# Kernel tuning notes

Measured on AMD Instinct MI355X. Metric: run time of the kernel, lower is better.

## Reference

```python
import jax, jax.numpy as jnp
import numpy as np

NUM_TASKS = 5
POOL = 5
R = 8
TOPK = 3
SCALE = 1.0  # module self.scale and forward scale arg, both 1
B, S, DIN, DOUT = 4, 4096, 1024, 1024


def setup_inputs() -> dict:
    key = jax.random.key(0)
    ks = jax.random.split(key, 5)
    inp = {
        "input": jax.random.normal(ks[0], (B, S, DIN), dtype=jnp.float32),
        "W": jax.random.normal(ks[1], (DOUT, DIN), dtype=jnp.float32) / np.sqrt(DIN),
        "lora_down": jax.random.normal(ks[2], (POOL, DIN, R), dtype=jnp.float32) / np.sqrt(DIN),
        "lora_up": jax.random.normal(ks[3], (POOL, R, DOUT), dtype=jnp.float32) / np.sqrt(R),
        "lora_route": jax.random.normal(ks[4], (NUM_TASKS, DIN, POOL), dtype=jnp.float32) * 0.02,
        "task_id": 4,
    }
    return inp


def reference(input, W, lora_down, lora_up, lora_route, task_id):
    # Eval branch (self.training == False), 1 <= task_id <= num_tasks.
    task_id = min(task_id, NUM_TASKS)
    k = min(task_id, TOPK)
    route = lora_route[1]                          # [DIN, POOL] (detach split is a no-op for fwd)
    input_mean = jnp.mean(input, axis=1)           # [B, DIN]
    lora_omegas = jnp.mean(input_mean @ route, axis=0)  # [POOL]
    sliced = lora_omegas[1:task_id + 1]            # source slices from 1
    G, I = jax.lax.top_k(sliced, k)                # indices used DIRECTLY (as in source)
    gate = jax.nn.softmax(G)                       # [k]
    # detached expert products (eval path detaches lora_down @ lora_up)
    dw = jax.lax.stop_gradient(
        jnp.einsum('kdr,kro->kdo', lora_down[I], lora_up[I]))  # [k, DIN, DOUT]
    # delta = sum_i gate[i] * SCALE * (input @ dw[i]); forward scale arg = 1
    delta = SCALE * jnp.einsum('k,bsd,kdo->bso', gate, input, dw)
    # delta_w_all[:B//2] = 0
    bmask = (jnp.arange(input.shape[0]) >= input.shape[0] // 2).astype(delta.dtype)
    delta = delta * bmask[:, None, None]
    return input @ W.T + delta
```

## Files before the change

### kernel.cpp

```cpp
#include <hip/hip_runtime.h>
#include <hip/hip_bf16.h>

typedef __attribute__((ext_vector_type(8))) __bf16 bf16x8;
typedef __attribute__((ext_vector_type(4))) __bf16 bf16x4;
typedef __attribute__((ext_vector_type(4))) float f32x4;

#define DIN 1024
#define DOUT 1024
#define BB 4
#define SS 4096
#define MROWS (BB*SS)
#define POOLN 5
#define RR 8
#define NTASKS 5
#define TOPKK 3

__global__ __launch_bounds__(256) void k1a_stream(const float* __restrict__ in,
                                                  __bf16* __restrict__ inB,
                                                  float* __restrict__ partial) {
    const int t = threadIdx.x;
    const int b = blockIdx.x;
    const int tid = b * 256 + t;
    const f32x4* __restrict__ inv = (const f32x4*)in;
    bf16x4* __restrict__ outv = (bf16x4*)inB;

    float s0 = 0.f, s1 = 0.f, s2 = 0.f, s3 = 0.f;
    size_t ia = (size_t)tid;
    size_t ib = (size_t)tid + 2097152;
    f32x4 ca = __builtin_nontemporal_load(&inv[ia]);
    f32x4 cb = __builtin_nontemporal_load(&inv[ib]);
#pragma unroll
    for (int i = 0; i < 4; ++i) {
        f32x4 na = ca, nb = cb;
        if (i < 3) {
            na = __builtin_nontemporal_load(&inv[ia + 524288]);
            nb = __builtin_nontemporal_load(&inv[ib + 524288]);
        }
        s0 += ca[0] + cb[0]; s1 += ca[1] + cb[1];
        s2 += ca[2] + cb[2]; s3 += ca[3] + cb[3];
        bf16x4 oa = { (__bf16)ca[0], (__bf16)ca[1], (__bf16)ca[2], (__bf16)ca[3] };
        bf16x4 ob = { (__bf16)cb[0], (__bf16)cb[1], (__bf16)cb[2], (__bf16)cb[3] };
        outv[ia] = oa;
        outv[ib] = ob;
        ca = na; cb = nb;
        ia += 524288; ib += 524288;
    }
    const int c0 = (t * 4) & (DIN - 1);
    f32x4 p = { s0, s1, s2, s3 };
    *(f32x4*)&partial[(size_t)b * DIN + c0] = p;
}

__global__ __launch_bounds__(256) void k1b_reduce(const float* __restrict__ partial,
                                                  float* __restrict__ partial2) {
    const int tid = blockIdx.x * 256 + threadIdx.x;
    const int c = tid & (DIN - 1);
    const int g = tid >> 10;
    float s = 0.f;
    const int r0 = g * 256;
#pragma unroll 8
    for (int r = r0; r < r0 + 256; ++r)
        s += partial[(size_t)r * DIN + c];
    partial2[(size_t)g * DIN + c] = s;
}

__global__ void k2_gate(const float* __restrict__ partial2,
                        const float* __restrict__ lroute,
                        const int* __restrict__ task_id_p,
                        float* __restrict__ gate, int* __restrict__ gidx) {
    __shared__ float red[4][POOLN];
    const int tix = threadIdx.x;
    const int w = tix >> 6, l = tix & 63;
    float part[POOLN] = {0.f, 0.f, 0.f, 0.f, 0.f};
    for (int d = w * 256 + l; d < w * 256 + 256; d += 64) {
        float cs = 0.f;
#pragma unroll
        for (int g = 0; g < 8; ++g) cs += partial2[g * DIN + d];
        cs *= (1.0f / (float)MROWS);
        const float* rp = &lroute[(size_t)1 * DIN * POOLN + (size_t)d * POOLN];
#pragma unroll
        for (int p = 0; p < POOLN; ++p) part[p] += cs * rp[p];
    }
#pragma unroll
    for (int p = 0; p < POOLN; ++p) {
        float v = part[p];
        for (int off = 32; off; off >>= 1) v += __shfl_down(v, off);
        if (l == 0) red[w][p] = v;
    }
    __syncthreads();
    if (tix == 0) {
#pragma unroll
        for (int p = 0; p < POOLN; ++p)
            part[p] = red[0][p] + red[1][p] + red[2][p] + red[3][p];
        int tid = *task_id_p;
        if (tid > NTASKS) tid = NTASKS;
        int L = tid < (POOLN - 1) ? tid : (POOLN - 1);
        int k = tid < TOPKK ? tid : TOPKK;
        float sl[POOLN];
        for (int j = 0; j < L; ++j) sl[j] = part[1 + j];
        float G[TOPKK]; int I[TOPKK];
        int used = 0;
        for (int j = 0; j < k; ++j) {
            int best = -1; float bv = 0.f;
            for (int i2 = 0; i2 < L; ++i2) {
                if (used & (1 << i2)) continue;
                if (best < 0 || sl[i2] > bv) { bv = sl[i2]; best = i2; }
            }
            used |= 1 << best; G[j] = bv; I[j] = best;
        }
        if (k > 0) {
            float m = G[0];
            float e[TOPKK]; float se = 0.f;
            for (int j = 0; j < k; ++j) { e[j] = expf(G[j] - m); se += e[j]; }
            for (int j = 0; j < k; ++j) { gate[j] = e[j] / se; gidx[j] = I[j]; }
        }
        for (int j = k; j < TOPKK; ++j) { gate[j] = 0.f; gidx[j] = 0; }
    }
}

__global__ __launch_bounds__(256) void k3_weights(const float* __restrict__ W,
                                                  const float* __restrict__ ldown,
                                                  const float* __restrict__ lup,
                                                  const float* __restrict__ gate,
                                                  const int* __restrict__ gidx,
                                                  __bf16* __restrict__ Wb0,
                                                  __bf16* __restrict__ Wb1) {
    const int o = blockIdx.x;
    const int t = threadIdx.x;
    float c[TOPKK][RR];
#pragma unroll
    for (int j = 0; j < TOPKK; ++j) {
        const float g = gate[j];
        const int   p = gidx[j];
#pragma unroll
        for (int r = 0; r < RR; ++r)
            c[j][r] = g * lup[(size_t)p * RR * DOUT + (size_t)r * DOUT + o];
    }
    const int d0 = t * 4;
    const float4 wv = *(const float4*)&W[(size_t)o * DIN + d0];
    float outv[4] = { wv.x, wv.y, wv.z, wv.w };
    float dwv[4]  = { 0.f, 0.f, 0.f, 0.f };
#pragma unroll
    for (int j = 0; j < TOPKK; ++j) {
        const int p = gidx[j];
#pragma unroll
        for (int dd = 0; dd < 4; ++dd) {
            const float4 da = *(const float4*)&ldown[(size_t)p * DIN * RR + (size_t)(d0 + dd) * RR];
            const float4 db = *(const float4*)&ldown[(size_t)p * DIN * RR + (size_t)(d0 + dd) * RR + 4];
            dwv[dd] += da.x * c[j][0] + da.y * c[j][1] + da.z * c[j][2] + da.w * c[j][3]
                     + db.x * c[j][4] + db.y * c[j][5] + db.z * c[j][6] + db.w * c[j][7];
        }
    }
    bf16x4 b0 = { (__bf16)outv[0], (__bf16)outv[1], (__bf16)outv[2], (__bf16)outv[3] };
    bf16x4 b1 = { (__bf16)(outv[0] + dwv[0]), (__bf16)(outv[1] + dwv[1]),
                  (__bf16)(outv[2] + dwv[2]), (__bf16)(outv[3] + dwv[3]) };
    *(bf16x4*)&Wb0[(size_t)o * DIN + d0] = b0;
    *(bf16x4*)&Wb1[(size_t)o * DIN + d0] = b1;
}

__global__ __launch_bounds__(512, 4) void k4_gemm(const __bf16* __restrict__ A,
                                                  const __bf16* __restrict__ B0,
                                                  const __bf16* __restrict__ B1,
                                                  float* __restrict__ C) {
    __shared__ ushort lds[36864];
    const int bid = blockIdx.x;
    const int xcd = bid & 7;
    const int idx = bid >> 3;
    const int tm  = xcd * 16 + (idx >> 2);
    const int tn  = idx & 3;
    const __bf16* __restrict__ Bt = (tm >= 64) ? B1 : B0;

    const int lane = threadIdx.x & 63;
    const int wid  = threadIdx.x >> 6;
    const int wm = wid >> 2, wn = wid & 3;

    const int rpl  = lane >> 3;
    const int sl   = (lane & 7) ^ rpl;
    const int srow = rpl * 2 + (sl >> 2);
    const int sc   = sl & 3;

    const char* gA = (const char*)A  + ((size_t)(tm*128 + wid*16 + srow)) * 2048 + sc * 16;
    const char* gB = (const char*)Bt + ((size_t)(tn*256 + wid*32 + srow)) * 2048 + sc * 16;
    const int ldsAst = wid * 512;
    const int ldsBst = 4096 + wid * 1024;

    const int rhalf = (lane & 15) >> 1;
    const int slot  = ((lane >> 4) + 4 * (lane & 1)) ^ rhalf;
    const int aoff  = (wm * 32 + rhalf) * 64 + slot * 8;
    const int boff  = 4096 + (wn * 32 + rhalf) * 64 + slot * 8;

    f32x4 acc[4][4];
#pragma unroll
    for (int i = 0; i < 4; ++i)
#pragma unroll
        for (int j = 0; j < 4; ++j) acc[i][j] = (f32x4){0.f, 0.f, 0.f, 0.f};

    auto stageSlab = [&](int s) {
        const int p = s % 3;
        const size_t kb = (size_t)s * 64;
        __builtin_amdgcn_global_load_lds(
            (const __attribute__((address_space(1))) void*)(gA + kb),
            (__attribute__((address_space(3))) void*)&lds[p * 12288 + ldsAst],
            16, 0, 0);
#pragma unroll
        for (int j = 0; j < 2; ++j) {
            __builtin_amdgcn_global_load_lds(
                (const __attribute__((address_space(1))) void*)(gB + (size_t)j * 32768 + kb),
                (__attribute__((address_space(3))) void*)&lds[p * 12288 + ldsBst + j * 512],
                16, 0, 0);
        }
    };

    auto computeSlab = [&](int s) {
        const int p = s % 3;
        const ushort* aB = &lds[p * 12288 + aoff];
        const ushort* bB = &lds[p * 12288 + boff];
        bf16x8 a[4], b[4];
#pragma unroll
        for (int mi = 0; mi < 4; ++mi) a[mi] = *(const bf16x8*)(aB + mi * 512);
#pragma unroll
        for (int ni = 0; ni < 4; ++ni) b[ni] = *(const bf16x8*)(bB + ni * 512);
        __builtin_amdgcn_s_setprio(1);
#pragma unroll
        for (int mi = 0; mi < 4; ++mi)
#pragma unroll
            for (int ni = 0; ni < 4; ++ni)
                acc[mi][ni] = __builtin_amdgcn_mfma_f32_16x16x32_bf16(
                    a[mi], b[ni], acc[mi][ni], 0, 0, 0);
        __builtin_amdgcn_s_setprio(0);
    };

    stageSlab(0); stageSlab(1);

#define K4_STEP(S, NSTR, DOSTAGE)                                     \
    {                                                                 \
        if (DOSTAGE) stageSlab((S) + 2);                              \
        asm volatile("s_waitcnt vmcnt(" NSTR ")" ::: "memory");       \
        __builtin_amdgcn_s_barrier();                                 \
        asm volatile("" ::: "memory");                                \
        computeSlab(S);                                               \
        asm volatile("" ::: "memory");                                \
        __builtin_amdgcn_s_barrier();                                 \
    }

#pragma unroll 1
    for (int s = 0; s < 30; ++s) K4_STEP(s, "6", true);
    K4_STEP(30, "3", false);
    K4_STEP(31, "0", false);
#undef K4_STEP

#pragma unroll
    for (int mi = 0; mi < 4; ++mi) {
#pragma unroll
        for (int r = 0; r < 4; ++r) {
            const int grow = tm * 128 + wm * 64 + mi * 16 + (lane >> 4) * 4 + r;
            float* cp = C + (size_t)grow * 1024 + tn * 256 + wn * 64 + (lane & 15);
#pragma unroll
            for (int ni = 0; ni < 4; ++ni) cp[ni * 16] = acc[mi][ni][r];
        }
    }
}

extern "C" void kernel_launch(void* const* d_in, const int* in_sizes, int n_in,
                              void* d_out, int out_size, void* d_ws, size_t ws_size,
                              hipStream_t stream) {
    const float* in     = (const float*)d_in[0];
    const float* W      = (const float*)d_in[1];
    const float* ldown  = (const float*)d_in[2];
    const float* lup    = (const float*)d_in[3];
    const float* lroute = (const float*)d_in[4];
    const int*   taskid = (const int*)d_in[5];
    float* out = (float*)d_out;

    __bf16* inB     = (__bf16*)d_ws;
    __bf16* Wb0     = inB + (size_t)MROWS * DIN;
    __bf16* Wb1     = Wb0 + (size_t)DOUT * DIN;
    float*  partial2= (float*)(Wb1 + (size_t)DOUT * DIN);
    float*  gate    = partial2 + 8 * DIN;
    int*    gidx    = (int*)(gate + TOPKK);

    float* partial = out;

    k1a_stream<<<2048, 256, 0, stream>>>(in, inB, partial);
    k1b_reduce<<<32, 256, 0, stream>>>(partial, partial2);
    k2_gate<<<1, 256, 0, stream>>>(partial2, lroute, taskid, gate, gidx);
    k3_weights<<<1024, 256, 0, stream>>>(W, ldown, lup, gate, gidx, Wb0, Wb1);
    k4_gemm<<<512, 512, 0, stream>>>(inB, Wb0, Wb1, out);
}
```

Before: 100.8 us.

## Fuse fp32-to-bf16 input conversion into GEMM A-tile loading

The separate streaming kernel no longer writes a bf16 copy of the input. The GEMM now loads fp32 A rows directly through registers, converts them to bf16 and writes them to LDS. The prologue kernel becomes a pure column-sum, and its partial sums move from the output buffer to workspace. This drops a 32MB bf16 write plus a 32MB read, at the cost of register-staged A loads, which replace the async global-to-LDS path, read twice the bytes of A inside the GEMM, and add an lgkmcnt wait.

```diff
diff --git a/kernel.cpp b/kernel.cpp
--- a/kernel.cpp
+++ b/kernel.cpp
@@ -15,35 +15,23 @@
 #define NTASKS 5
 #define TOPKK 3
 
-__global__ __launch_bounds__(256) void k1a_stream(const float* __restrict__ in,
-                                                  __bf16* __restrict__ inB,
-                                                  float* __restrict__ partial) {
+__global__ __launch_bounds__(256) void kA_colsum(const float* __restrict__ in,
+                                                 float* __restrict__ partial) {
     const int t = threadIdx.x;
     const int b = blockIdx.x;
-    const int tid = b * 256 + t;
+    const int idx0 = b * 256 + t;
     const f32x4* __restrict__ inv = (const f32x4*)in;
-    bf16x4* __restrict__ outv = (bf16x4*)inB;
 
     float s0 = 0.f, s1 = 0.f, s2 = 0.f, s3 = 0.f;
-    size_t ia = (size_t)tid;
-    size_t ib = (size_t)tid + 2097152;
-    f32x4 ca = __builtin_nontemporal_load(&inv[ia]);
-    f32x4 cb = __builtin_nontemporal_load(&inv[ib]);
-#pragma unroll
-    for (int i = 0; i < 4; ++i) {
-        f32x4 na = ca, nb = cb;
-        if (i < 3) {
-            na = __builtin_nontemporal_load(&inv[ia + 524288]);
-            nb = __builtin_nontemporal_load(&inv[ib + 524288]);
-        }
-        s0 += ca[0] + cb[0]; s1 += ca[1] + cb[1];
-        s2 += ca[2] + cb[2]; s3 += ca[3] + cb[3];
-        bf16x4 oa = { (__bf16)ca[0], (__bf16)ca[1], (__bf16)ca[2], (__bf16)ca[3] };
-        bf16x4 ob = { (__bf16)cb[0], (__bf16)cb[1], (__bf16)cb[2], (__bf16)cb[3] };
-        outv[ia] = oa;
-        outv[ib] = ob;
-        ca = na; cb = nb;
-        ia += 524288; ib += 524288;
+    size_t idx = idx0;
+    f32x4 cur = inv[idx];
+#pragma unroll
+    for (int i = 0; i < 8; ++i) {
+        f32x4 nxt = cur;
+        if (i < 7) nxt = inv[idx + 524288];
+        s0 += cur[0]; s1 += cur[1]; s2 += cur[2]; s3 += cur[3];
+        cur = nxt;
+        idx += 524288;
     }
     const int c0 = (t * 4) & (DIN - 1);
     f32x4 p = { s0, s1, s2, s3 };
@@ -157,7 +145,7 @@
     *(bf16x4*)&Wb1[(size_t)o * DIN + d0] = b1;
 }
 
-__global__ __launch_bounds__(512, 4) void k4_gemm(const __bf16* __restrict__ A,
+__global__ __launch_bounds__(512, 4) void k4_gemm(const float* __restrict__ A,
                                                   const __bf16* __restrict__ B0,
                                                   const __bf16* __restrict__ B1,
                                                   float* __restrict__ C) {
@@ -169,18 +157,23 @@
     const int tn  = idx & 3;
     const __bf16* __restrict__ Bt = (tm >= 64) ? B1 : B0;
 
-    const int lane = threadIdx.x & 63;
-    const int wid  = threadIdx.x >> 6;
+    const int tix  = threadIdx.x;
+    const int lane = tix & 63;
+    const int wid  = tix >> 6;
     const int wm = wid >> 2, wn = wid & 3;
+
+    const int ar = tix >> 2;
+    const int ac = tix & 3;
+    const f32x4* __restrict__ pA = (const f32x4*)(A + ((size_t)(tm * 128 + ar)) * 1024 + ac * 8);
+    const int awrp  = tix >> 3;
+    const int awslot= ((tix & 3) + 4 * ((tix >> 2) & 1)) ^ (awrp & 7);
+    const int awoff = awrp * 64 + awslot * 8;
 
     const int rpl  = lane >> 3;
     const int sl   = (lane & 7) ^ rpl;
     const int srow = rpl * 2 + (sl >> 2);
     const int sc   = sl & 3;
-
-    const char* gA = (const char*)A  + ((size_t)(tm*128 + wid*16 + srow)) * 2048 + sc * 16;
     const char* gB = (const char*)Bt + ((size_t)(tn*256 + wid*32 + srow)) * 2048 + sc * 16;
-    const int ldsAst = wid * 512;
     const int ldsBst = 4096 + wid * 1024;
 
     const int rhalf = (lane & 15) >> 1;
@@ -194,13 +187,9 @@
 #pragma unroll
         for (int j = 0; j < 4; ++j) acc[i][j] = (f32x4){0.f, 0.f, 0.f, 0.f};
 
-    auto stageSlab = [&](int s) {
+    auto issueB = [&](int s) {
         const int p = s % 3;
         const size_t kb = (size_t)s * 64;
-        __builtin_amdgcn_global_load_lds(
-            (const __attribute__((address_space(1))) void*)(gA + kb),
-            (__attribute__((address_space(3))) void*)&lds[p * 12288 + ldsAst],
-            16, 0, 0);
 #pragma unroll
         for (int j = 0; j < 2; ++j) {
             __builtin_amdgcn_global_load_lds(
@@ -210,6 +199,13 @@
         }
     };
 
+    auto writeA = [&](int s, f32x4 a0, f32x4 a1) {
+        const int p = s % 3;
+        bf16x8 v = { (__bf16)a0[0], (__bf16)a0[1], (__bf16)a0[2], (__bf16)a0[3],
+                     (__bf16)a1[0], (__bf16)a1[1], (__bf16)a1[2], (__bf16)a1[3] };
+        *(bf16x8*)&lds[p * 12288 + awoff] = v;
+    };
+
     auto computeSlab = [&](int s) {
         const int p = s % 3;
         const ushort* aB = &lds[p * 12288 + aoff];
@@ -229,24 +225,33 @@
         __builtin_amdgcn_s_setprio(0);
     };
 
-    stageSlab(0); stageSlab(1);
-
-#define K4_STEP(S, NSTR, DOSTAGE)                                     \
-    {                                                                 \
-        if (DOSTAGE) stageSlab((S) + 2);                              \
-        asm volatile("s_waitcnt vmcnt(" NSTR ")" ::: "memory");       \
-        __builtin_amdgcn_s_barrier();                                 \
-        asm volatile("" ::: "memory");                                \
-        computeSlab(S);                                               \
-        asm volatile("" ::: "memory");                                \
-        __builtin_amdgcn_s_barrier();                                 \
-    }
+    f32x4 pa0 = pA[0], pa1 = pA[1];
+    issueB(0);
+    f32x4 na0 = pA[8], na1 = pA[9];
+    issueB(1);
+    asm volatile("s_waitcnt vmcnt(6)" ::: "memory");
+    writeA(0, pa0, pa1);
 
 #pragma unroll 1
-    for (int s = 0; s < 30; ++s) K4_STEP(s, "6", true);
-    K4_STEP(30, "3", false);
-    K4_STEP(31, "0", false);
-#undef K4_STEP
+    for (int s = 0; s < 32; ++s) {
+        if (s < 31) {
+            asm volatile("s_waitcnt vmcnt(2)" ::: "memory");
+            writeA(s + 1, na0, na1);
+        } else {
+            asm volatile("s_waitcnt vmcnt(0)" ::: "memory");
+        }
+        if (s < 30) {
+            na0 = pA[(size_t)(s + 2) * 8];
+            na1 = pA[(size_t)(s + 2) * 8 + 1];
+            issueB(s + 2);
+        }
+        asm volatile("s_waitcnt lgkmcnt(0)" ::: "memory");
+        __builtin_amdgcn_s_barrier();
+        asm volatile("" ::: "memory");
+        computeSlab(s);
+        asm volatile("" ::: "memory");
+        __builtin_amdgcn_s_barrier();
+    }
 
 #pragma unroll
     for (int mi = 0; mi < 4; ++mi) {
@@ -271,18 +276,16 @@
     const int*   taskid = (const int*)d_in[5];
     float* out = (float*)d_out;
 
-    __bf16* inB     = (__bf16*)d_ws;
-    __bf16* Wb0     = inB + (size_t)MROWS * DIN;
+    __bf16* Wb0     = (__bf16*)d_ws;
     __bf16* Wb1     = Wb0 + (size_t)DOUT * DIN;
     float*  partial2= (float*)(Wb1 + (size_t)DOUT * DIN);
     float*  gate    = partial2 + 8 * DIN;
     int*    gidx    = (int*)(gate + TOPKK);
-
-    float* partial = out;
-
-    k1a_stream<<<2048, 256, 0, stream>>>(in, inB, partial);
+    float*  partial = (float*)(gidx + 64);
+
+    kA_colsum<<<2048, 256, 0, stream>>>(in, partial);
     k1b_reduce<<<32, 256, 0, stream>>>(partial, partial2);
     k2_gate<<<1, 256, 0, stream>>>(partial2, lroute, taskid, gate, gidx);
     k3_weights<<<1024, 256, 0, stream>>>(W, ldown, lup, gate, gidx, Wb0, Wb1);
-    k4_gemm<<<512, 512, 0, stream>>>(inB, Wb0, Wb1, out);
-}
+    k4_gemm<<<512, 512, 0, stream>>>(in, Wb0, Wb1, out);
+}
```

New measurement: 94.41 us. -6.4%, faster.
